# Optimization experiments

Measured on AMD Instinct MI355X. Metric: run time of the kernel, lower is better.

Reference implementation:

```python
import jax, jax.numpy as jnp
import numpy as np

B, N, H, HEADS = 8, 1024, 512, 4  # batch graphs, nodes/graph, graph_hsz, attention heads
R = 64  # relations per graph (passthrough)


def setup_inputs() -> dict:
    key = jax.random.key(0)
    k1, k2, k3, k4, k5, k6, k7 = jax.random.split(key, 7)
    adjs = jax.random.randint(k1, (B, N, N), 0, 2, dtype=jnp.int32)  # 0 => masked
    nodes = jax.random.normal(k2, (B, N, H), dtype=jnp.float32)
    triples = jax.random.normal(k3, (B, R, H), dtype=jnp.float32)   # unused in gat path
    relations = jax.random.normal(k4, (B, R, H), dtype=jnp.float32)  # passthrough
    node_num = jnp.full((B,), N, dtype=jnp.int32)  # all graphs full => no padding branch
    s = 1.0 / np.sqrt(H)
    Wq = (jax.random.normal(k5, (H, H), dtype=jnp.float32) * s)
    Wk = (jax.random.normal(k6, (H, H), dtype=jnp.float32) * s)
    Wv = (jax.random.normal(k7, (H, H), dtype=jnp.float32) * s)
    return {"adjs": adjs, "triples": triples, "nodes": nodes, "node_num": node_num,
            "relations": relations, "Wq": Wq, "Wk": Wk, "Wv": Wv}


def reference(adjs, triples, nodes, node_num, relations, Wq, Wk, Wv):
    b, n, h = nodes.shape
    dk = h // HEADS
    scale = 1.0 / jnp.sqrt(jnp.float32(h))  # torch divides by sqrt(key_dim)=sqrt(H)

    def to_heads(x, W):  # [B,N,H] -> [B,heads,N,dk]; matches split(dim=-1)+stack
        return (x @ W).reshape(b, n, HEADS, dk).transpose(0, 2, 1, 3)

    Q = to_heads(nodes, Wq)
    K = to_heads(nodes, Wk)
    V = to_heads(nodes, Wv)
    att = jnp.einsum('bhnd,bhmd->bhnm', Q, K) * scale
    att = jnp.where((adjs == 0)[:, None, :, :], -jnp.inf, att)
    p = jax.nn.softmax(att, axis=-1)  # dropout_p = blockdrop = 0.0 => identity
    out = jnp.einsum('bhnm,bhmd->bhnd', p, V)
    out = out.transpose(0, 2, 1, 3).reshape(b, n, h)  # concat heads along feature dim
    out = jax.nn.relu(out)
    return (out, relations)
```

## Files before the change

### kernel.cpp

```cpp
#include <hip/hip_runtime.h>
#include <stdint.h>

typedef __attribute__((ext_vector_type(4))) float f32x4;
typedef __attribute__((ext_vector_type(16))) float f32x16;
typedef __attribute__((ext_vector_type(8))) short bf16x8;
typedef unsigned long long ull;

#define GLB_AS const __attribute__((address_space(1)))
#define LDS_AS __attribute__((address_space(3)))

__device__ __forceinline__ short f2bf(float f) {
    union { float f; unsigned u; } x; x.f = f;
    unsigned r = x.u + 0x7FFFu + ((x.u >> 16) & 1u);
    return (short)(r >> 16);
}

__global__ void k_pre(const float* __restrict__ nodes, short* __restrict__ nodes_bf,
                      const float* __restrict__ Wq, const float* __restrict__ Wk,
                      const float* __restrict__ Wv, short* __restrict__ WT,
                      const int* __restrict__ adjs, unsigned* __restrict__ packed) {
    int bi = blockIdx.x, tid = threadIdx.x;
    if (bi < 2048) {
        int i = (bi * 256 + tid) * 8;
        float4 a = *(const float4*)(nodes + i);
        float4 b = *(const float4*)(nodes + i + 4);
        bf16x8 v;
        v[0] = f2bf(a.x); v[1] = f2bf(a.y); v[2] = f2bf(a.z); v[3] = f2bf(a.w);
        v[4] = f2bf(b.x); v[5] = f2bf(b.y); v[6] = f2bf(b.z); v[7] = f2bf(b.w);
        *(bf16x8*)(nodes_bf + i) = v;
    } else if (bi < 5120) {
        int g = (bi - 2048) * 256 + tid;
        int j = g >> 9, k = g & 511;
        int w = j >> 9, n = j & 511;
        const float* W = (w == 0) ? Wq : (w == 1) ? Wk : Wv;
        WT[g] = f2bf(W[k * 512 + n]);
    } else {
        int g = (bi - 5120) * 256 + tid;
        int wv = g >> 6, lane = g & 63;
        ull m = __ballot(adjs[(size_t)wv * 64 + lane] != 0);
        if (lane == 0) *(ull*)(packed + (size_t)wv * 2) = m;
    }
}

__global__ __launch_bounds__(256) void k_gemm_qkv(const short* __restrict__ A,
                                                  const short* __restrict__ WT,
                                                  short* __restrict__ C) {
    __shared__ short Asm[2][128 * 32];
    __shared__ short Bsm[2][128 * 32];
    const int tid = threadIdx.x;
    const int l = tid & 63, w = tid >> 6;
    const int wr = w >> 1, wc = w & 1;
    const int c16 = l & 15, g = l >> 4;
    const int wg = blockIdx.x;
    const int swz = (wg & 7) * 96 + (wg >> 3);
    const int row0 = (swz / 12) * 128, n0 = (swz % 12) * 128;
    f32x4 acc[4][4] = {};

    auto stage = [&](int kt, int bsel) {
        const int k0 = kt * 32;
#pragma unroll
        for (int i = 0; i < 2; ++i) {
            int ch = tid + 256 * i;
            int r = ch >> 2, gc = ch & 3;
            __builtin_amdgcn_global_load_lds((GLB_AS unsigned*)(A + (row0 + r) * 512 + k0 + 8 * gc),
                                             (LDS_AS unsigned*)(&Asm[bsel][ch * 8]), 16, 0, 0);
            __builtin_amdgcn_global_load_lds((GLB_AS unsigned*)(WT + (n0 + r) * 512 + k0 + 8 * gc),
                                             (LDS_AS unsigned*)(&Bsm[bsel][ch * 8]), 16, 0, 0);
        }
    };

    stage(0, 0);
    asm volatile("s_waitcnt vmcnt(0)" ::: "memory");
    __syncthreads();

    for (int kt = 0; kt < 16; ++kt) {
        const int cur = kt & 1;
        if (kt < 15) stage(kt + 1, cur ^ 1);
        bf16x8 af[4], bfr[4];
#pragma unroll
        for (int mf = 0; mf < 4; ++mf)
            af[mf] = *(const bf16x8*)&Asm[cur][(wr * 64 + mf * 16 + c16) * 32 + 8 * g];
#pragma unroll
        for (int nf = 0; nf < 4; ++nf)
            bfr[nf] = *(const bf16x8*)&Bsm[cur][(wc * 64 + nf * 16 + c16) * 32 + 8 * g];
#pragma unroll
        for (int mf = 0; mf < 4; ++mf)
#pragma unroll
            for (int nf = 0; nf < 4; ++nf)
                acc[mf][nf] = __builtin_amdgcn_mfma_f32_16x16x32_bf16(af[mf], bfr[nf], acc[mf][nf], 0, 0, 0);
        asm volatile("s_waitcnt vmcnt(0)" ::: "memory");
        __syncthreads();
    }
#pragma unroll
    for (int mf = 0; mf < 4; ++mf)
#pragma unroll
        for (int nf = 0; nf < 4; ++nf) {
            const float cs = (n0 + wc * 64 + nf * 16 < 512) ? 0.06375872022286384f : 1.0f;
#pragma unroll
            for (int r = 0; r < 4; ++r) {
                int row = row0 + wr * 64 + mf * 16 + 4 * g + r;
                int col = n0 + wc * 64 + nf * 16 + c16;
                C[row * 1536 + col] = f2bf(acc[mf][nf][r] * cs);
            }
        }
}

__global__ __launch_bounds__(256) void k_mid(const short* __restrict__ QKV, short* __restrict__ Vt2,
                                             short* __restrict__ Kt2,
                                             const float* __restrict__ rel_in, float* __restrict__ rel_out) {
    const int bi = blockIdx.x, t = threadIdx.x;
    if (bi >= 1280) {
        int g = (bi - 1280) * 256 + t;
        int c = g & 63, m = (g >> 6) & 1023, b = g >> 16;
        int h = c >> 4, khc = c & 15;
        bf16x8 v = *(const bf16x8*)(QKV + (size_t)(b * 1024 + m) * 1536 + 512 + c * 8);
        *(bf16x8*)(Kt2 + ((((size_t)(b * 4 + h) * 32 + (m >> 5)) * 16 + khc) * 32 + (m & 31)) * 8) = v;
        return;
    }
    if (bi >= 1024) {
        int i = ((bi - 1024) * 256 + t) * 4;
        *(float4*)(rel_out + i) = *(const float4*)(rel_in + i);
        return;
    }
    __shared__ short tile[64 * 65];
    const int b = bi >> 7, n0 = ((bi >> 3) & 15) * 64, d0 = (bi & 7) * 64;
#pragma unroll
    for (int i = 0; i < 16; ++i) {
        int idx = t + 256 * i;
        int nn = idx >> 6, dd = idx & 63;
        tile[nn * 65 + dd] = QKV[(b * 1024 + n0 + nn) * 1536 + 1024 + d0 + dd];
    }
    __syncthreads();
#pragma unroll
    for (int i = 0; i < 2; ++i) {
        int c = t + 256 * i;
        int dd = c >> 3, nl = (c & 7) * 8;
        int dg = d0 + dd;
        int h = dg >> 7, dh = dg & 127;
        bf16x8 v;
#pragma unroll
        for (int e = 0; e < 8; ++e)
            v[e] = tile[(nl + e) * 65 + dd];
        *(bf16x8*)(Vt2 + ((((size_t)(b * 4 + h)) * 128 + ((n0 + nl) >> 3)) * 128 + dh) * 8) = v;
    }
}

__global__ __launch_bounds__(512, 2) void k_attn(const short* __restrict__ QKV, const short* __restrict__ Kt2,
                                                 const short* __restrict__ Vt2,
                                                 const unsigned* __restrict__ packed, float* __restrict__ out) {
    __shared__ char smem[66560];
    float* OshA = (float*)smem;
    float* OshB = (float*)(smem + 32768);
    float* lsh  = (float*)(smem + 65536);
    const int bh = blockIdx.x;
    const int b = bh >> 2, h = bh & 3;
    const int q0 = blockIdx.y * 64;
    const int tid = threadIdx.x, l = tid & 63, wid = tid >> 6;
    const int mg = wid >> 1, wq = wid & 1;
    const int l31 = l & 31, hi = l >> 5;
    const int qw = q0 + wq * 32;

    bf16x8 aq[8];
    const short* Qb = QKV + (size_t)(b * 1024 + qw + l31) * 1536 + h * 128;
#pragma unroll
    for (int kk = 0; kk < 8; ++kk)
        aq[kk] = *(const bf16x8*)(Qb + kk * 16 + hi * 8);

    f32x16 acc[4] = {};
    float l_lane = 0.f;

    const short* K2b = Kt2 + (size_t)(b * 4 + h) * 131072;
    const short* V2b = Vt2 + (size_t)(b * 4 + h) * 131072;
    const unsigned* adjw = packed + (size_t)(b * 1024 + qw + l31) * 32 + mg * 8;

    bf16x8 kcur[8], knxt[8], vcur[8];
    {
        const int mt = mg * 8;
#pragma unroll
        for (int kk = 0; kk < 8; ++kk)
            kcur[kk] = *(const bf16x8*)(K2b + ((size_t)(mt * 16 + 2 * kk + hi) * 32 + l31) * 8);
    }
    unsigned mcur = adjw[0];

#pragma unroll
    for (int t = 0; t < 8; ++t) {
        const int mc0 = mg * 32 + t * 4;
#pragma unroll
        for (int ks = 0; ks < 2; ++ks)
#pragma unroll
            for (int dd = 0; dd < 4; ++dd)
                vcur[ks * 4 + dd] = *(const bf16x8*)(V2b + ((size_t)(mc0 + 2 * ks + hi) * 128 + dd * 32 + l31) * 8);
        unsigned mnx = 0;
        if (t < 7) {
            const int mt = mg * 8 + t + 1;
#pragma unroll
            for (int kk = 0; kk < 8; ++kk)
                knxt[kk] = *(const bf16x8*)(K2b + ((size_t)(mt * 16 + 2 * kk + hi) * 32 + l31) * 8);
            mnx = adjw[t + 1];
        }

        f32x16 s = (f32x16)0.f;
        __builtin_amdgcn_s_setprio(1);
#pragma unroll
        for (int kk = 0; kk < 8; ++kk)
            s = __builtin_amdgcn_mfma_f32_32x32x16_bf16(kcur[kk], aq[kk], s, 0, 0, 0);
        __builtin_amdgcn_s_setprio(0);

        unsigned pk[4][2];
        const unsigned mshift = mcur >> (4 * hi);
        float lt = 0.f;
#pragma unroll
        for (int j = 0; j < 4; ++j) {
            float p[4];
#pragma unroll
            for (int r = 0; r < 4; ++r) {
                float e = __builtin_amdgcn_exp2f(s[4 * j + r]);
                p[r] = ((mshift >> (8 * j + r)) & 1u) ? e : 0.f;
            }
            lt += (p[0] + p[1]) + (p[2] + p[3]);
            asm("v_cvt_pk_bf16_f32 %0, %1, %2" : "=v"(pk[j][0]) : "v"(p[0]), "v"(p[1]));
            asm("v_cvt_pk_bf16_f32 %0, %1, %2" : "=v"(pk[j][1]) : "v"(p[2]), "v"(p[3]));
        }
        l_lane += lt;

        union fragu { unsigned u[4]; bf16x8 v; };
        fragu frag[2];
#pragma unroll
        for (int kh = 0; kh < 2; ++kh) {
            unsigned a0 = pk[2 * kh][0], a1 = pk[2 * kh][1];
            unsigned b0 = pk[2 * kh + 1][0], b1 = pk[2 * kh + 1][1];
            unsigned rx0 = (unsigned)__shfl_xor((int)a0, 32);
            unsigned rx1 = (unsigned)__shfl_xor((int)a1, 32);
            unsigned rx2 = (unsigned)__shfl_xor((int)b0, 32);
            unsigned rx3 = (unsigned)__shfl_xor((int)b1, 32);
            fragu f;
            f.u[0] = hi ? rx2 : a0;
            f.u[1] = hi ? rx3 : a1;
            f.u[2] = hi ? b0 : rx0;
            f.u[3] = hi ? b1 : rx1;
            frag[kh] = f;
        }

        __builtin_amdgcn_s_setprio(1);
#pragma unroll
        for (int ks = 0; ks < 2; ++ks)
#pragma unroll
            for (int dd = 0; dd < 4; ++dd)
                acc[dd] = __builtin_amdgcn_mfma_f32_32x32x16_bf16(frag[ks].v, vcur[ks * 4 + dd], acc[dd], 0, 0, 0);
        __builtin_amdgcn_s_setprio(0);

#pragma unroll
        for (int kk = 0; kk < 8; ++kk) kcur[kk] = knxt[kk];
        mcur = mnx;
    }

    l_lane += __shfl_xor(l_lane, 32);
    if (hi == 0) lsh[mg * 64 + wq * 32 + l31] = l_lane;

    if (mg == 1 || mg == 3) {
        float* O = (mg == 1) ? OshA : OshB;
#pragma unroll
        for (int dd = 0; dd < 4; ++dd)
#pragma unroll
            for (int j = 0; j < 4; ++j)
#pragma unroll
                for (int r = 0; r < 4; ++r) {
                    int qrow = wq * 32 + r + 8 * j + 4 * hi;
                    O[qrow * 128 + dd * 32 + l31] = acc[dd][4 * j + r];
                }
    }
    __syncthreads();
    if (mg == 0 || mg == 2) {
        const float* O = (mg == 0) ? OshA : OshB;
#pragma unroll
        for (int dd = 0; dd < 4; ++dd)
#pragma unroll
            for (int j = 0; j < 4; ++j)
#pragma unroll
                for (int r = 0; r < 4; ++r) {
                    int qrow = wq * 32 + r + 8 * j + 4 * hi;
                    acc[dd][4 * j + r] += O[qrow * 128 + dd * 32 + l31];
                }
    }
    __syncthreads();
    if (mg == 2) {
#pragma unroll
        for (int dd = 0; dd < 4; ++dd)
#pragma unroll
            for (int j = 0; j < 4; ++j)
#pragma unroll
                for (int r = 0; r < 4; ++r) {
                    int qrow = wq * 32 + r + 8 * j + 4 * hi;
                    OshA[qrow * 128 + dd * 32 + l31] = acc[dd][4 * j + r];
                }
    }
    __syncthreads();
    if (mg == 0) {
        float invq[16];
#pragma unroll
        for (int j = 0; j < 4; ++j)
#pragma unroll
            for (int r = 0; r < 4; ++r) {
                int qrow = wq * 32 + r + 8 * j + 4 * hi;
                invq[4 * j + r] = 1.f / (lsh[qrow] + lsh[64 + qrow] + lsh[128 + qrow] + lsh[192 + qrow]);
            }
#pragma unroll
        for (int dd = 0; dd < 4; ++dd)
#pragma unroll
            for (int j = 0; j < 4; ++j)
#pragma unroll
                for (int r = 0; r < 4; ++r) {
                    int qrow = wq * 32 + r + 8 * j + 4 * hi;
                    float o = (acc[dd][4 * j + r] + OshA[qrow * 128 + dd * 32 + l31]) * invq[4 * j + r];
                    out[(size_t)(b * 1024 + q0 + qrow) * 512 + h * 128 + dd * 32 + l31] = fmaxf(o, 0.f);
                }
    }
}

extern "C" void kernel_launch(void* const* d_in, const int* in_sizes, int n_in,
                              void* d_out, int out_size, void* d_ws, size_t ws_size,
                              hipStream_t stream) {
    const int*   adjs      = (const int*)d_in[0];
    const float* nodes     = (const float*)d_in[2];
    const float* relations = (const float*)d_in[4];
    const float* Wq        = (const float*)d_in[5];
    const float* Wk        = (const float*)d_in[6];
    const float* Wv        = (const float*)d_in[7];

    char* ws = (char*)d_ws;
    short* nodes_bf   = (short*)(ws);
    short* WT         = (short*)(ws + 8388608);
    short* QKV        = (short*)(ws + 9961472);
    short* Vt2        = (short*)(ws + 35127296);
    unsigned* adjpack = (unsigned*)(ws + 43515904);
    short* Kt2        = (short*)(ws + 44564480);

    float* out     = (float*)d_out;
    float* out_rel = out + 4194304;

    k_pre<<<dim3(37888), dim3(256), 0, stream>>>(nodes, nodes_bf, Wq, Wk, Wv, WT, adjs, adjpack);
    k_gemm_qkv<<<dim3(768), dim3(256), 0, stream>>>(nodes_bf, WT, QKV);
    k_mid<<<dim3(3328), dim3(256), 0, stream>>>(QKV, Vt2, Kt2, relations, out_rel);
    k_attn<<<dim3(32, 16), dim3(512), 0, stream>>>(QKV, Kt2, Vt2, adjpack, out);
}
```

Before: 85.14 us.

## Shrink attention blocks to 32 queries and drop K double-buffering

The attention kernel now uses 256-thread blocks that each handle 32 query rows instead of 64, which doubles the grid and halves shared memory per block. The software-pipelined prefetch of the next K tile is removed, so K is loaded inside each iteration. The adjacency mask words are loaded up front as two vector loads rather than one word per iteration. The aim is to cut register and LDS pressure so more waves fit per CU and to spread work across more blocks. The cost is exposed K load latency and twice as many block launches, each re-reading the K and V data.

```diff
diff --git a/kernel.cpp b/kernel.cpp
--- a/kernel.cpp
+++ b/kernel.cpp
@@ -4,6 +4,7 @@
 typedef __attribute__((ext_vector_type(4))) float f32x4;
 typedef __attribute__((ext_vector_type(16))) float f32x16;
 typedef __attribute__((ext_vector_type(8))) short bf16x8;
+typedef __attribute__((ext_vector_type(4))) unsigned uint4v;
 typedef unsigned long long ull;
 
 #define GLB_AS const __attribute__((address_space(1)))
@@ -145,23 +146,22 @@
     }
 }
 
-__global__ __launch_bounds__(512, 2) void k_attn(const short* __restrict__ QKV, const short* __restrict__ Kt2,
+__global__ __launch_bounds__(256, 2) void k_attn(const short* __restrict__ QKV, const short* __restrict__ Kt2,
                                                  const short* __restrict__ Vt2,
                                                  const unsigned* __restrict__ packed, float* __restrict__ out) {
-    __shared__ char smem[66560];
+    __shared__ char smem[33280];
     float* OshA = (float*)smem;
-    float* OshB = (float*)(smem + 32768);
-    float* lsh  = (float*)(smem + 65536);
+    float* OshB = (float*)(smem + 16384);
+    float* lsh  = (float*)(smem + 32768);
     const int bh = blockIdx.x;
     const int b = bh >> 2, h = bh & 3;
-    const int q0 = blockIdx.y * 64;
-    const int tid = threadIdx.x, l = tid & 63, wid = tid >> 6;
-    const int mg = wid >> 1, wq = wid & 1;
+    const int q0 = blockIdx.y * 32;
+    const int tid = threadIdx.x, l = tid & 63;
+    const int mg = tid >> 6;
     const int l31 = l & 31, hi = l >> 5;
-    const int qw = q0 + wq * 32;
 
     bf16x8 aq[8];
-    const short* Qb = QKV + (size_t)(b * 1024 + qw + l31) * 1536 + h * 128;
+    const short* Qb = QKV + (size_t)(b * 1024 + q0 + l31) * 1536 + h * 128;
 #pragma unroll
     for (int kk = 0; kk < 8; ++kk)
         aq[kk] = *(const bf16x8*)(Qb + kk * 16 + hi * 8);
@@ -171,33 +171,26 @@
 
     const short* K2b = Kt2 + (size_t)(b * 4 + h) * 131072;
     const short* V2b = Vt2 + (size_t)(b * 4 + h) * 131072;
-    const unsigned* adjw = packed + (size_t)(b * 1024 + qw + l31) * 32 + mg * 8;
-
-    bf16x8 kcur[8], knxt[8], vcur[8];
-    {
-        const int mt = mg * 8;
+    const unsigned* adjw = packed + (size_t)(b * 1024 + q0 + l31) * 32 + mg * 8;
+
+    unsigned mall[8];
+#pragma unroll
+    for (int i = 0; i < 2; ++i)
+        *(uint4v*)(mall + 4 * i) = *(const uint4v*)(adjw + 4 * i);
+
+#pragma unroll
+    for (int t = 0; t < 8; ++t) {
+        const int mt = mg * 8 + t;
+        bf16x8 kcur[8], vcur[8];
 #pragma unroll
         for (int kk = 0; kk < 8; ++kk)
             kcur[kk] = *(const bf16x8*)(K2b + ((size_t)(mt * 16 + 2 * kk + hi) * 32 + l31) * 8);
-    }
-    unsigned mcur = adjw[0];
-
-#pragma unroll
-    for (int t = 0; t < 8; ++t) {
         const int mc0 = mg * 32 + t * 4;
 #pragma unroll
         for (int ks = 0; ks < 2; ++ks)
 #pragma unroll
             for (int dd = 0; dd < 4; ++dd)
                 vcur[ks * 4 + dd] = *(const bf16x8*)(V2b + ((size_t)(mc0 + 2 * ks + hi) * 128 + dd * 32 + l31) * 8);
-        unsigned mnx = 0;
-        if (t < 7) {
-            const int mt = mg * 8 + t + 1;
-#pragma unroll
-            for (int kk = 0; kk < 8; ++kk)
-                knxt[kk] = *(const bf16x8*)(K2b + ((size_t)(mt * 16 + 2 * kk + hi) * 32 + l31) * 8);
-            mnx = adjw[t + 1];
-        }
 
         f32x16 s = (f32x16)0.f;
         __builtin_amdgcn_s_setprio(1);
@@ -207,7 +200,7 @@
         __builtin_amdgcn_s_setprio(0);
 
         unsigned pk[4][2];
-        const unsigned mshift = mcur >> (4 * hi);
+        const unsigned mshift = mall[t] >> (4 * hi);
         float lt = 0.f;
 #pragma unroll
         for (int j = 0; j < 4; ++j) {
@@ -248,14 +241,10 @@
             for (int dd = 0; dd < 4; ++dd)
                 acc[dd] = __builtin_amdgcn_mfma_f32_32x32x16_bf16(frag[ks].v, vcur[ks * 4 + dd], acc[dd], 0, 0, 0);
         __builtin_amdgcn_s_setprio(0);
-
-#pragma unroll
-        for (int kk = 0; kk < 8; ++kk) kcur[kk] = knxt[kk];
-        mcur = mnx;
     }
 
     l_lane += __shfl_xor(l_lane, 32);
-    if (hi == 0) lsh[mg * 64 + wq * 32 + l31] = l_lane;
+    if (hi == 0) lsh[mg * 32 + l31] = l_lane;
 
     if (mg == 1 || mg == 3) {
         float* O = (mg == 1) ? OshA : OshB;
@@ -265,7 +254,7 @@
             for (int j = 0; j < 4; ++j)
 #pragma unroll
                 for (int r = 0; r < 4; ++r) {
-                    int qrow = wq * 32 + r + 8 * j + 4 * hi;
+                    int qrow = r + 8 * j + 4 * hi;
                     O[qrow * 128 + dd * 32 + l31] = acc[dd][4 * j + r];
                 }
     }
@@ -278,7 +267,7 @@
             for (int j = 0; j < 4; ++j)
 #pragma unroll
                 for (int r = 0; r < 4; ++r) {
-                    int qrow = wq * 32 + r + 8 * j + 4 * hi;
+                    int qrow = r + 8 * j + 4 * hi;
                     acc[dd][4 * j + r] += O[qrow * 128 + dd * 32 + l31];
                 }
     }
@@ -290,7 +279,7 @@
             for (int j = 0; j < 4; ++j)
 #pragma unroll
                 for (int r = 0; r < 4; ++r) {
-                    int qrow = wq * 32 + r + 8 * j + 4 * hi;
+                    int qrow = r + 8 * j + 4 * hi;
                     OshA[qrow * 128 + dd * 32 + l31] = acc[dd][4 * j + r];
                 }
     }
@@ -301,8 +290,8 @@
         for (int j = 0; j < 4; ++j)
 #pragma unroll
             for (int r = 0; r < 4; ++r) {
-                int qrow = wq * 32 + r + 8 * j + 4 * hi;
-                invq[4 * j + r] = 1.f / (lsh[qrow] + lsh[64 + qrow] + lsh[128 + qrow] + lsh[192 + qrow]);
+                int qrow = r + 8 * j + 4 * hi;
+                invq[4 * j + r] = 1.f / (lsh[qrow] + lsh[32 + qrow] + lsh[64 + qrow] + lsh[96 + qrow]);
             }
 #pragma unroll
         for (int dd = 0; dd < 4; ++dd)
@@ -310,7 +299,7 @@
             for (int j = 0; j < 4; ++j)
 #pragma unroll
                 for (int r = 0; r < 4; ++r) {
-                    int qrow = wq * 32 + r + 8 * j + 4 * hi;
+                    int qrow = r + 8 * j + 4 * hi;
                     float o = (acc[dd][4 * j + r] + OshA[qrow * 128 + dd * 32 + l31]) * invq[4 * j + r];
                     out[(size_t)(b * 1024 + q0 + qrow) * 512 + h * 128 + dd * 32 + l31] = fmaxf(o, 0.f);
                 }
@@ -341,5 +330,5 @@
     k_pre<<<dim3(37888), dim3(256), 0, stream>>>(nodes, nodes_bf, Wq, Wk, Wv, WT, adjs, adjpack);
     k_gemm_qkv<<<dim3(768), dim3(256), 0, stream>>>(nodes_bf, WT, QKV);
     k_mid<<<dim3(3328), dim3(256), 0, stream>>>(QKV, Vt2, Kt2, relations, out_rel);
-    k_attn<<<dim3(32, 16), dim3(512), 0, stream>>>(QKV, Kt2, Vt2, adjpack, out);
-}
+    k_attn<<<dim3(32, 32), dim3(256), 0, stream>>>(QKV, Kt2, Vt2, adjpack, out);
+}
```

Result: no change. 84.72 us (-0.5%).
